# Kernel tuning notes

Hardware: AMD Instinct MI355X
Metric: run time of the kernel (lower is better)

## Reference

```python
import jax, jax.numpy as jnp
import numpy as np

GAMMA = 2.0  # init arg gamma
EPS = 1e-8   # torch F.cosine_similarity eps


def setup_inputs() -> dict:
    key = jax.random.key(0)
    k1, k2, k3 = jax.random.split(key, 3)
    B, C, H, W_ = 4, 256, 64, 64
    x = jax.random.normal(k1, (B, C, H, W_), dtype=jnp.float32)
    # 1x1 conv weight [out_c, in_c] and bias
    W = jax.random.normal(k2, (C, C), dtype=jnp.float32) * (1.0 / np.sqrt(C))
    b = jax.random.normal(k3, (C,), dtype=jnp.float32) * 0.01
    return {"x": x, "W": W, "b": b}


def reference(x, W, b):
    B, C, H, W_ = x.shape
    N = H * W_
    xf = x.reshape(B, C, N)                                    # [B,C,N]
    # cosine similarity across channel dim, with torch-style eps clamp
    norm = jnp.maximum(jnp.sqrt(jnp.sum(xf * xf, axis=1)), EPS)  # [B,N]
    xn = xf / norm[:, None, :]                                  # [B,C,N]
    sim = jnp.einsum('bcn,bcm->bnm', xn, xn)                    # [B,N,N]
    sim = jax.nn.relu(sim) ** GAMMA
    # 1x1 conv = per-pixel channel mixing
    t = jnp.einsum('oc,bchw->bohw', W, x) + b[None, :, None, None]
    tf = t.reshape(B, C, N)                                     # [B,C,N]
    # einsum 'b x y h w, b c h w -> b c x y'
    out = jnp.einsum('bnm,bcm->bcn', sim, tf)
    return out.reshape(B, C, H, W_)
```

## Files before the change

kernel.cpp:

```cpp
#include <hip/hip_runtime.h>
#include <stdint.h>

#define CC 256
#define NN 4096

typedef __attribute__((ext_vector_type(8))) short short8;
typedef __attribute__((ext_vector_type(4))) float floatx4;
typedef __attribute__((ext_vector_type(4))) unsigned int uint4v;
typedef __attribute__((ext_vector_type(2))) unsigned int uint2v;

__device__ __forceinline__ unsigned short f2bf(float f) {
    unsigned int u = __builtin_bit_cast(unsigned int, f);
    u = (u + 0x7FFFu + ((u >> 16) & 1u)) >> 16;
    return (unsigned short)u;
}

__device__ __forceinline__ floatx4 mfma16(short8 a, short8 b, floatx4 c) {
    return __builtin_amdgcn_mfma_f32_16x16x32_bf16(a, b, c, 0, 0, 0);
}

__device__ __forceinline__ int swz8(int row, int g) {
    return row * 256 + (((g ^ (row & 7)) & 31) << 3);
}

__global__ __launch_bounds__(256) void k_wcast(const float* __restrict__ Wm,
                                               unsigned short* __restrict__ wF) {
    int idx = blockIdx.x * 256 + threadIdx.x;
    int f = idx >> 6, lane = idx & 63;
    int ct = f >> 3, kk = f & 7;
    int l15 = lane & 15, q = lane >> 4;
    const float* src = Wm + (size_t)(16 * ct + l15) * CC + 32 * kk + 8 * q;
    floatx4 a = *(const floatx4*)src;
    floatx4 c = *(const floatx4*)(src + 4);
    unsigned int w0 = f2bf(a[0]) | ((unsigned int)f2bf(a[1]) << 16);
    unsigned int w1 = f2bf(a[2]) | ((unsigned int)f2bf(a[3]) << 16);
    unsigned int w2 = f2bf(c[0]) | ((unsigned int)f2bf(c[1]) << 16);
    unsigned int w3 = f2bf(c[2]) | ((unsigned int)f2bf(c[3]) << 16);
    uint4v p = {w0, w1, w2, w3};
    *(uint4v*)(wF + (size_t)f * 512 + lane * 8) = p;
}

__global__ __launch_bounds__(256) void k_trans(const float* __restrict__ x,
                                               unsigned short* __restrict__ xT,
                                               float* __restrict__ psum) {
    int blk = blockIdx.x;
    int b  = blk >> 8;
    int cc = (blk >> 6) & 3;
    int nc = blk & 63;
    int c0 = cc << 6, n0 = nc << 6;
    __shared__ float tile[64][65];
    __shared__ float red[4][64];
    int t = threadIdx.x;
    {
        int c   = t >> 2;
        int nn4 = (t & 3) << 4;
        const float* src = x + (size_t)(b * CC + c0 + c) * NN + n0 + nn4;
        #pragma unroll
        for (int j = 0; j < 16; j += 4) {
            floatx4 v = *(const floatx4*)(src + j);
            tile[c][nn4 + j + 0] = v[0];
            tile[c][nn4 + j + 1] = v[1];
            tile[c][nn4 + j + 2] = v[2];
            tile[c][nn4 + j + 3] = v[3];
        }
    }
    __syncthreads();
    {
        int n  = t >> 2;
        int ci = (t & 3) << 4;
        unsigned short* dst = xT + (size_t)(b * NN + n0 + n) * CC + c0 + ci;
        unsigned int w[8];
        #pragma unroll
        for (int j = 0; j < 8; ++j) {
            unsigned int lo = f2bf(tile[ci + 2 * j][n]);
            unsigned int hi = f2bf(tile[ci + 2 * j + 1][n]);
            w[j] = lo | (hi << 16);
        }
        uint4v w0 = {w[0], w[1], w[2], w[3]};
        uint4v w1 = {w[4], w[5], w[6], w[7]};
        *(uint4v*)(dst)     = w0;
        *(uint4v*)(dst + 8) = w1;
    }
    {
        int n  = t & 63;
        int cq = t >> 6;
        float ss = 0.f;
        #pragma unroll
        for (int i = 0; i < 16; ++i) {
            float v = tile[cq * 16 + i][n];
            ss = fmaf(v, v, ss);
        }
        red[cq][n] = ss;
    }
    __syncthreads();
    if (t < 64) {
        float s = red[0][t] + red[1][t] + red[2][t] + red[3][t];
        psum[((size_t)(b * 64 + nc) * 64 + t) * 4 + cc] = s;
    }
}

__global__ __launch_bounds__(256) void k_inv(const float* __restrict__ psum,
                                             float* __restrict__ invn) {
    int i = blockIdx.x * 256 + threadIdx.x;
    floatx4 p = *(const floatx4*)(psum + (size_t)i * 4);
    float ss = (p[0] + p[1]) + (p[2] + p[3]);
    invn[i] = 1.f / fmaxf(sqrtf(ss), 1e-8f);
}

__global__ __launch_bounds__(256) void k_gfrag(const unsigned short* __restrict__ xT,
                                               unsigned short* __restrict__ xG) {
    int blk = blockIdx.x;
    int b = blk >> 6, mt = blk & 63;
    __shared__ unsigned short tile[64 * 264];
    int t = threadIdx.x;
    const unsigned short* src = xT + (size_t)(b * NN + mt * 64) * CC;
    #pragma unroll
    for (int j = 0; j < 8; ++j) {
        int idx = j * 256 + t;
        int row = idx >> 5, g = idx & 31;
        uint4v v = *(const uint4v*)(src + (size_t)row * CC + g * 8);
        *(uint4v*)(tile + row * 264 + g * 8) = v;
    }
    __syncthreads();
    unsigned short* dst = xG + (size_t)(b * 64 + mt) * 16 * 1024;
    int lane = t & 63, l15 = lane & 15, q = lane >> 4;
    #pragma unroll
    for (int cc2 = 0; cc2 < 4; ++cc2) {
        int cct = (t >> 6) * 4 + cc2;
        #pragma unroll
        for (int kk2 = 0; kk2 < 2; ++kk2) {
            unsigned int w[4];
            #pragma unroll
            for (int j2 = 0; j2 < 4; ++j2) {
                unsigned int lo = tile[(32 * kk2 + 8 * q + 2 * j2) * 264 + 16 * cct + l15];
                unsigned int hi = tile[(32 * kk2 + 8 * q + 2 * j2 + 1) * 264 + 16 * cct + l15];
                w[j2] = lo | (hi << 16);
            }
            uint4v p = {w[0], w[1], w[2], w[3]};
            *(uint4v*)(dst + cct * 1024 + kk2 * 512 + lane * 8) = p;
        }
    }
}

__global__ __launch_bounds__(512, 2) void k_fused(
        const unsigned short* __restrict__ xT,
        const unsigned short* __restrict__ xG,
        const unsigned short* __restrict__ wF,
        const float* __restrict__ bias,
        const float* __restrict__ invn,
        float* __restrict__ out) {
    int blk = blockIdx.x;
    int b  = blk >> 6;
    int n0 = (blk & 63) << 6;
    int t  = threadIdx.x;
    int wv = t >> 6;
    int l15 = t & 15, q = (t & 63) >> 4;
    int ms = wv & 3;
    int np = wv >> 2;

    __shared__ unsigned short xm[64 * 256];
    __shared__ unsigned short pbuf[4][16 * 72];
    __shared__ unsigned short zbuf[64 * 264];
    __shared__ float spbuf2[4][64];

    const unsigned short* xTb = xT + (size_t)b * NN * CC;
    const unsigned short* xGb = xG + (size_t)b * 64 * 16 * 1024;
    const float* invb = invn + b * NN;

    short8 aq[2][8];
    #pragma unroll
    for (int s = 0; s < 2; ++s) {
        const unsigned short* p = xTb + (size_t)(n0 + 16 * (2 * np + s) + l15) * CC + q * 8;
        #pragma unroll
        for (int kk = 0; kk < 8; ++kk) aq[s][kk] = *(const short8*)(p + kk * 32);
    }
    float invq[2][4];
    #pragma unroll
    for (int s = 0; s < 2; ++s)
        #pragma unroll
        for (int i = 0; i < 4; ++i)
            invq[s][i] = invb[n0 + 16 * (2 * np + s) + q * 4 + i];

    floatx4 zero4 = {0.f, 0.f, 0.f, 0.f};
    floatx4 Zacc[2][4];
    #pragma unroll
    for (int ci = 0; ci < 2; ++ci)
        #pragma unroll
        for (int nqs = 0; nqs < 4; ++nqs) Zacc[ci][nqs] = zero4;
    float csum[2][4];
    #pragma unroll
    for (int s = 0; s < 2; ++s)
        #pragma unroll
        for (int i = 0; i < 4; ++i) csum[s][i] = 0.f;

    int srow = t >> 5;
    int sg   = t & 31;
    uint4v gx[4];
    #pragma unroll
    for (int j = 0; j < 4; ++j)
        gx[j] = *(const uint4v*)(xTb + (size_t)(j * 16 + srow) * CC + sg * 8);
    #pragma unroll
    for (int j = 0; j < 4; ++j)
        *(uint4v*)(xm + swz8(j * 16 + srow, sg)) = gx[j];
    __syncthreads();

    for (int it = 0; it < 64; ++it) {
        int m0 = it << 6;
        int m1 = (it < 63 ? (it + 1) : 63) << 6;
        #pragma unroll
        for (int j = 0; j < 4; ++j)
            gx[j] = *(const uint4v*)(xTb + (size_t)(m1 + j * 16 + srow) * CC + sg * 8);
        short8 xg[2][2];
        #pragma unroll
        for (int ci = 0; ci < 2; ++ci)
            #pragma unroll
            for (int kk2 = 0; kk2 < 2; ++kk2) {
                int cct = wv + 8 * ci;
                xg[ci][kk2] = *(const short8*)(xGb + (size_t)(it * 16 + cct) * 1024
                                               + kk2 * 512 + (t & 63) * 8);
            }
        float invm = invb[m0 + 16 * ms + l15];

        short8 bq[8];
        #pragma unroll
        for (int kk = 0; kk < 8; ++kk)
            bq[kk] = *(const short8*)(xm + swz8(16 * ms + l15, kk * 4 + q));
        floatx4 s0a = zero4, s0b = zero4, s1a = zero4, s1b = zero4;
        #pragma unroll
        for (int kk = 0; kk < 8; kk += 2) {
            s0a = mfma16(aq[0][kk],     bq[kk],     s0a);
            s1a = mfma16(aq[1][kk],     bq[kk],     s1a);
            s0b = mfma16(aq[0][kk + 1], bq[kk + 1], s0b);
            s1b = mfma16(aq[1][kk + 1], bq[kk + 1], s1b);
        }
        #pragma unroll
        for (int s = 0; s < 2; ++s) {
            floatx4 sv = (s == 0) ? (s0a + s0b) : (s1a + s1b);
            unsigned short* pw = &pbuf[2 * np + s][16 * ms + l15];
            #pragma unroll
            for (int i = 0; i < 4; ++i) {
                float v = sv[i] * (invq[s][i] * invm);
                v = fmaxf(v, 0.f);
                v = v * v;
                csum[s][i] += v;
                pw[(q * 4 + i) * 72] = f2bf(v);
            }
        }
        asm volatile("s_waitcnt lgkmcnt(0)\n\ts_barrier" ::: "memory");

        #pragma unroll
        for (int kk2 = 0; kk2 < 2; ++kk2)
            #pragma unroll
            for (int nqs = 0; nqs < 4; ++nqs) {
                short8 pbf = *(const short8*)(&pbuf[nqs][l15 * 72 + kk2 * 32 + q * 8]);
                Zacc[0][nqs] = mfma16(xg[0][kk2], pbf, Zacc[0][nqs]);
                Zacc[1][nqs] = mfma16(xg[1][kk2], pbf, Zacc[1][nqs]);
            }
        #pragma unroll
        for (int j = 0; j < 4; ++j)
            *(uint4v*)(xm + swz8(j * 16 + srow, sg)) = gx[j];
        asm volatile("s_waitcnt lgkmcnt(0)\n\ts_barrier" ::: "memory");
    }

    #pragma unroll
    for (int mask = 1; mask < 16; mask <<= 1)
        #pragma unroll
        for (int s = 0; s < 2; ++s)
            #pragma unroll
            for (int i = 0; i < 4; ++i)
                csum[s][i] += __shfl_xor(csum[s][i], mask, 64);

    __syncthreads();
    #pragma unroll
    for (int ci = 0; ci < 2; ++ci) {
        int cct = wv + 8 * ci;
        #pragma unroll
        for (int nqs = 0; nqs < 4; ++nqs)
            #pragma unroll
            for (int i = 0; i < 4; ++i)
                zbuf[(16 * nqs + l15) * 264 + 16 * cct + 4 * q + i] = f2bf(Zacc[ci][nqs][i]);
    }
    if (l15 == 0) {
        #pragma unroll
        for (int s = 0; s < 2; ++s)
            #pragma unroll
            for (int i = 0; i < 4; ++i)
                spbuf2[ms][16 * (2 * np + s) + 4 * q + i] = csum[s][i];
    }
    __syncthreads();

    float svals[4];
    #pragma unroll
    for (int nqs = 0; nqs < 4; ++nqs)
        svals[nqs] = spbuf2[0][16 * nqs + l15] + spbuf2[1][16 * nqs + l15]
                   + spbuf2[2][16 * nqs + l15] + spbuf2[3][16 * nqs + l15];

    float* ob = out + (size_t)b * CC * NN;
    floatx4 oa[2][4];
    #pragma unroll
    for (int ci = 0; ci < 2; ++ci) {
        int ct = wv + 8 * ci;
        floatx4 bv = *(const floatx4*)(bias + 16 * ct + 4 * q);
        #pragma unroll
        for (int nqs = 0; nqs < 4; ++nqs)
            #pragma unroll
            for (int i = 0; i < 4; ++i) oa[ci][nqs][i] = bv[i] * svals[nqs];
    }
    #pragma unroll
    for (int kk = 0; kk < 8; ++kk) {
        short8 wf0 = *(const short8*)(wF + (size_t)(wv * 8 + kk) * 512 + (t & 63) * 8);
        short8 wf1 = *(const short8*)(wF + (size_t)((wv + 8) * 8 + kk) * 512 + (t & 63) * 8);
        #pragma unroll
        for (int nqs = 0; nqs < 4; ++nqs) {
            short8 zf = *(const short8*)(&zbuf[(16 * nqs + l15) * 264 + 32 * kk + 8 * q]);
            oa[0][nqs] = mfma16(wf0, zf, oa[0][nqs]);
            oa[1][nqs] = mfma16(wf1, zf, oa[1][nqs]);
        }
    }
    #pragma unroll
    for (int ci = 0; ci < 2; ++ci) {
        int ct = wv + 8 * ci;
        #pragma unroll
        for (int nqs = 0; nqs < 4; ++nqs)
            #pragma unroll
            for (int i = 0; i < 4; ++i)
                ob[(size_t)(16 * ct + 4 * q + i) * NN + n0 + 16 * nqs + l15] = oa[ci][nqs][i];
    }
}

extern "C" void kernel_launch(void* const* d_in, const int* in_sizes, int n_in,
                              void* d_out, int out_size, void* d_ws, size_t ws_size,
                              hipStream_t stream) {
    const float* x    = (const float*)d_in[0];
    const float* Wm   = (const float*)d_in[1];
    const float* bias = (const float*)d_in[2];
    float* out = (float*)d_out;

    char* ws = (char*)d_ws;
    float* psum         = (float*)ws;
    float* invn         = (float*)(ws + 262144);
    unsigned short* xT  = (unsigned short*)(ws + 262144 + 65536);
    unsigned short* wF  = (unsigned short*)(ws + 262144 + 65536 + 8388608);
    unsigned short* xG  = (unsigned short*)(ws + 262144 + 65536 + 8388608 + 131072);

    k_wcast<<<32,   256, 0, stream>>>(Wm, wF);
    k_trans<<<1024, 256, 0, stream>>>(x, xT, psum);
    k_inv  <<<64,   256, 0, stream>>>(psum, invn);
    k_gfrag<<<256,  256, 0, stream>>>(xT, xG);
    k_fused<<<256,  512, 0, stream>>>(xT, xG, wF, bias, invn, out);
}
```

Measured before the change: 169.9 us.

## Emit MFMA-fragment layouts directly from transpose kernel and drop LDS staging loop

The transpose kernel now writes x in two pre-swizzled MFMA fragment layouts (xB for the similarity operand, xG for the aggregation operand), which removes the separate gfrag kernel. The weight cast is merged with the inverse-norm kernel, cutting five launches to three. In the fused kernel the per-iteration key tile is read straight from global memory in fragment order rather than staged through swizzled LDS, and pbuf is double-buffered. Together these remove one barrier and the LDS round trip per iteration. The cost is more global and L2 traffic for the key fragments and a larger workspace.

```diff
diff --git a/kernel.cpp b/kernel.cpp
--- a/kernel.cpp
+++ b/kernel.cpp
@@ -7,7 +7,6 @@
 typedef __attribute__((ext_vector_type(8))) short short8;
 typedef __attribute__((ext_vector_type(4))) float floatx4;
 typedef __attribute__((ext_vector_type(4))) unsigned int uint4v;
-typedef __attribute__((ext_vector_type(2))) unsigned int uint2v;
 
 __device__ __forceinline__ unsigned short f2bf(float f) {
     unsigned int u = __builtin_bit_cast(unsigned int, f);
@@ -19,29 +18,10 @@
     return __builtin_amdgcn_mfma_f32_16x16x32_bf16(a, b, c, 0, 0, 0);
 }
 
-__device__ __forceinline__ int swz8(int row, int g) {
-    return row * 256 + (((g ^ (row & 7)) & 31) << 3);
-}
-
-__global__ __launch_bounds__(256) void k_wcast(const float* __restrict__ Wm,
-                                               unsigned short* __restrict__ wF) {
-    int idx = blockIdx.x * 256 + threadIdx.x;
-    int f = idx >> 6, lane = idx & 63;
-    int ct = f >> 3, kk = f & 7;
-    int l15 = lane & 15, q = lane >> 4;
-    const float* src = Wm + (size_t)(16 * ct + l15) * CC + 32 * kk + 8 * q;
-    floatx4 a = *(const floatx4*)src;
-    floatx4 c = *(const floatx4*)(src + 4);
-    unsigned int w0 = f2bf(a[0]) | ((unsigned int)f2bf(a[1]) << 16);
-    unsigned int w1 = f2bf(a[2]) | ((unsigned int)f2bf(a[3]) << 16);
-    unsigned int w2 = f2bf(c[0]) | ((unsigned int)f2bf(c[1]) << 16);
-    unsigned int w3 = f2bf(c[2]) | ((unsigned int)f2bf(c[3]) << 16);
-    uint4v p = {w0, w1, w2, w3};
-    *(uint4v*)(wF + (size_t)f * 512 + lane * 8) = p;
-}
 
 __global__ __launch_bounds__(256) void k_trans(const float* __restrict__ x,
-                                               unsigned short* __restrict__ xT,
+                                               unsigned short* __restrict__ xB,
+                                               unsigned short* __restrict__ xG,
                                                float* __restrict__ psum) {
     int blk = blockIdx.x;
     int b  = blk >> 8;
@@ -65,21 +45,32 @@
         }
     }
     __syncthreads();
-    {
-        int n  = t >> 2;
-        int ci = (t & 3) << 4;
-        unsigned short* dst = xT + (size_t)(b * NN + n0 + n) * CC + c0 + ci;
-        unsigned int w[8];
-        #pragma unroll
-        for (int j = 0; j < 8; ++j) {
-            unsigned int lo = f2bf(tile[ci + 2 * j][n]);
-            unsigned int hi = f2bf(tile[ci + 2 * j + 1][n]);
+    int g = t >> 6, lane = t & 63, l15 = lane & 15, q = lane >> 4;
+    #pragma unroll
+    for (int kkl = 0; kkl < 2; ++kkl) {
+        unsigned int w[4];
+        #pragma unroll
+        for (int j = 0; j < 4; ++j) {
+            unsigned int lo = f2bf(tile[32 * kkl + 8 * q + 2 * j][16 * g + l15]);
+            unsigned int hi = f2bf(tile[32 * kkl + 8 * q + 2 * j + 1][16 * g + l15]);
             w[j] = lo | (hi << 16);
         }
-        uint4v w0 = {w[0], w[1], w[2], w[3]};
-        uint4v w1 = {w[4], w[5], w[6], w[7]};
-        *(uint4v*)(dst)     = w0;
-        *(uint4v*)(dst + 8) = w1;
+        uint4v p = {w[0], w[1], w[2], w[3]};
+        *(uint4v*)(xB + ((size_t)(b * 256 + (n0 >> 4) + g) * 8 + (c0 >> 5) + kkl) * 512
+                   + lane * 8) = p;
+    }
+    #pragma unroll
+    for (int kk2 = 0; kk2 < 2; ++kk2) {
+        unsigned int w[4];
+        #pragma unroll
+        for (int j = 0; j < 4; ++j) {
+            unsigned int lo = f2bf(tile[16 * g + l15][32 * kk2 + 8 * q + 2 * j]);
+            unsigned int hi = f2bf(tile[16 * g + l15][32 * kk2 + 8 * q + 2 * j + 1]);
+            w[j] = lo | (hi << 16);
+        }
+        uint4v p = {w[0], w[1], w[2], w[3]};
+        *(uint4v*)(xG + (size_t)(b * 64 + nc) * 16 * 1024
+                   + ((size_t)((c0 >> 4) + g)) * 1024 + kk2 * 512 + lane * 8) = p;
     }
     {
         int n  = t & 63;
@@ -99,51 +90,36 @@
     }
 }
 
-__global__ __launch_bounds__(256) void k_inv(const float* __restrict__ psum,
-                                             float* __restrict__ invn) {
-    int i = blockIdx.x * 256 + threadIdx.x;
-    floatx4 p = *(const floatx4*)(psum + (size_t)i * 4);
-    float ss = (p[0] + p[1]) + (p[2] + p[3]);
-    invn[i] = 1.f / fmaxf(sqrtf(ss), 1e-8f);
-}
-
-__global__ __launch_bounds__(256) void k_gfrag(const unsigned short* __restrict__ xT,
-                                               unsigned short* __restrict__ xG) {
-    int blk = blockIdx.x;
-    int b = blk >> 6, mt = blk & 63;
-    __shared__ unsigned short tile[64 * 264];
+__global__ __launch_bounds__(256) void k_invwcast(const float* __restrict__ psum,
+                                                  float* __restrict__ invn,
+                                                  const float* __restrict__ Wm,
+                                                  unsigned short* __restrict__ wF) {
+    int bid = blockIdx.x;
     int t = threadIdx.x;
-    const unsigned short* src = xT + (size_t)(b * NN + mt * 64) * CC;
-    #pragma unroll
-    for (int j = 0; j < 8; ++j) {
-        int idx = j * 256 + t;
-        int row = idx >> 5, g = idx & 31;
-        uint4v v = *(const uint4v*)(src + (size_t)row * CC + g * 8);
-        *(uint4v*)(tile + row * 264 + g * 8) = v;
-    }
-    __syncthreads();
-    unsigned short* dst = xG + (size_t)(b * 64 + mt) * 16 * 1024;
-    int lane = t & 63, l15 = lane & 15, q = lane >> 4;
-    #pragma unroll
-    for (int cc2 = 0; cc2 < 4; ++cc2) {
-        int cct = (t >> 6) * 4 + cc2;
-        #pragma unroll
-        for (int kk2 = 0; kk2 < 2; ++kk2) {
-            unsigned int w[4];
-            #pragma unroll
-            for (int j2 = 0; j2 < 4; ++j2) {
-                unsigned int lo = tile[(32 * kk2 + 8 * q + 2 * j2) * 264 + 16 * cct + l15];
-                unsigned int hi = tile[(32 * kk2 + 8 * q + 2 * j2 + 1) * 264 + 16 * cct + l15];
-                w[j2] = lo | (hi << 16);
-            }
-            uint4v p = {w[0], w[1], w[2], w[3]};
-            *(uint4v*)(dst + cct * 1024 + kk2 * 512 + lane * 8) = p;
-        }
+    if (bid < 64) {
+        int i = bid * 256 + t;
+        floatx4 p = *(const floatx4*)(psum + (size_t)i * 4);
+        float ss = (p[0] + p[1]) + (p[2] + p[3]);
+        invn[i] = 1.f / fmaxf(sqrtf(ss), 1e-8f);
+    } else {
+        int idx = (bid - 64) * 256 + t;
+        int f = idx >> 6, lane = idx & 63;
+        int ct = f >> 3, kk = f & 7;
+        int l15 = lane & 15, q = lane >> 4;
+        const float* src = Wm + (size_t)(16 * ct + l15) * CC + 32 * kk + 8 * q;
+        floatx4 a = *(const floatx4*)src;
+        floatx4 c = *(const floatx4*)(src + 4);
+        unsigned int w0 = f2bf(a[0]) | ((unsigned int)f2bf(a[1]) << 16);
+        unsigned int w1 = f2bf(a[2]) | ((unsigned int)f2bf(a[3]) << 16);
+        unsigned int w2 = f2bf(c[0]) | ((unsigned int)f2bf(c[1]) << 16);
+        unsigned int w3 = f2bf(c[2]) | ((unsigned int)f2bf(c[3]) << 16);
+        uint4v p = {w0, w1, w2, w3};
+        *(uint4v*)(wF + (size_t)f * 512 + lane * 8) = p;
     }
 }
 
 __global__ __launch_bounds__(512, 2) void k_fused(
-        const unsigned short* __restrict__ xT,
+        const unsigned short* __restrict__ xB,
         const unsigned short* __restrict__ xG,
         const unsigned short* __restrict__ wF,
         const float* __restrict__ bias,
@@ -153,27 +129,26 @@
     int b  = blk >> 6;
     int n0 = (blk & 63) << 6;
     int t  = threadIdx.x;
-    int wv = t >> 6;
-    int l15 = t & 15, q = (t & 63) >> 4;
+    int wv = t >> 6, lane = t & 63;
+    int l15 = lane & 15, q = lane >> 4;
     int ms = wv & 3;
     int np = wv >> 2;
 
-    __shared__ unsigned short xm[64 * 256];
-    __shared__ unsigned short pbuf[4][16 * 72];
+    __shared__ unsigned short pbuf[2][64 * 72];
     __shared__ unsigned short zbuf[64 * 264];
     __shared__ float spbuf2[4][64];
 
-    const unsigned short* xTb = xT + (size_t)b * NN * CC;
+    const unsigned short* xBb = xB + (size_t)b * 256 * 8 * 512;
     const unsigned short* xGb = xG + (size_t)b * 64 * 16 * 1024;
     const float* invb = invn + b * NN;
 
     short8 aq[2][8];
     #pragma unroll
-    for (int s = 0; s < 2; ++s) {
-        const unsigned short* p = xTb + (size_t)(n0 + 16 * (2 * np + s) + l15) * CC + q * 8;
-        #pragma unroll
-        for (int kk = 0; kk < 8; ++kk) aq[s][kk] = *(const short8*)(p + kk * 32);
-    }
+    for (int s = 0; s < 2; ++s)
+        #pragma unroll
+        for (int kk = 0; kk < 8; ++kk)
+            aq[s][kk] = *(const short8*)(xBb
+                + ((size_t)((n0 >> 4) + 2 * np + s) * 8 + kk) * 512 + lane * 8);
     float invq[2][4];
     #pragma unroll
     for (int s = 0; s < 2; ++s)
@@ -193,38 +168,23 @@
         #pragma unroll
         for (int i = 0; i < 4; ++i) csum[s][i] = 0.f;
 
-    int srow = t >> 5;
-    int sg   = t & 31;
-    uint4v gx[4];
-    #pragma unroll
-    for (int j = 0; j < 4; ++j)
-        gx[j] = *(const uint4v*)(xTb + (size_t)(j * 16 + srow) * CC + sg * 8);
-    #pragma unroll
-    for (int j = 0; j < 4; ++j)
-        *(uint4v*)(xm + swz8(j * 16 + srow, sg)) = gx[j];
-    __syncthreads();
-
     for (int it = 0; it < 64; ++it) {
+        unsigned short* pb = pbuf[it & 1];
         int m0 = it << 6;
-        int m1 = (it < 63 ? (it + 1) : 63) << 6;
-        #pragma unroll
-        for (int j = 0; j < 4; ++j)
-            gx[j] = *(const uint4v*)(xTb + (size_t)(m1 + j * 16 + srow) * CC + sg * 8);
+        short8 bq[8];
+        #pragma unroll
+        for (int kk = 0; kk < 8; ++kk)
+            bq[kk] = *(const short8*)(xBb
+                + ((size_t)(it * 4 + ms) * 8 + kk) * 512 + lane * 8);
         short8 xg[2][2];
         #pragma unroll
         for (int ci = 0; ci < 2; ++ci)
             #pragma unroll
-            for (int kk2 = 0; kk2 < 2; ++kk2) {
-                int cct = wv + 8 * ci;
-                xg[ci][kk2] = *(const short8*)(xGb + (size_t)(it * 16 + cct) * 1024
-                                               + kk2 * 512 + (t & 63) * 8);
-            }
+            for (int kk2 = 0; kk2 < 2; ++kk2)
+                xg[ci][kk2] = *(const short8*)(xGb
+                    + (size_t)(it * 16 + wv + 8 * ci) * 1024 + kk2 * 512 + lane * 8);
         float invm = invb[m0 + 16 * ms + l15];
 
-        short8 bq[8];
-        #pragma unroll
-        for (int kk = 0; kk < 8; ++kk)
-            bq[kk] = *(const short8*)(xm + swz8(16 * ms + l15, kk * 4 + q));
         floatx4 s0a = zero4, s0b = zero4, s1a = zero4, s1b = zero4;
         #pragma unroll
         for (int kk = 0; kk < 8; kk += 2) {
@@ -236,7 +196,7 @@
         #pragma unroll
         for (int s = 0; s < 2; ++s) {
             floatx4 sv = (s == 0) ? (s0a + s0b) : (s1a + s1b);
-            unsigned short* pw = &pbuf[2 * np + s][16 * ms + l15];
+            unsigned short* pw = pb + (16 * (2 * np + s)) * 72 + 16 * ms + l15;
             #pragma unroll
             for (int i = 0; i < 4; ++i) {
                 float v = sv[i] * (invq[s][i] * invm);
@@ -252,14 +212,11 @@
         for (int kk2 = 0; kk2 < 2; ++kk2)
             #pragma unroll
             for (int nqs = 0; nqs < 4; ++nqs) {
-                short8 pbf = *(const short8*)(&pbuf[nqs][l15 * 72 + kk2 * 32 + q * 8]);
+                short8 pbf = *(const short8*)(pb + (16 * nqs + l15) * 72
+                                              + kk2 * 32 + q * 8);
                 Zacc[0][nqs] = mfma16(xg[0][kk2], pbf, Zacc[0][nqs]);
                 Zacc[1][nqs] = mfma16(xg[1][kk2], pbf, Zacc[1][nqs]);
             }
-        #pragma unroll
-        for (int j = 0; j < 4; ++j)
-            *(uint4v*)(xm + swz8(j * 16 + srow, sg)) = gx[j];
-        asm volatile("s_waitcnt lgkmcnt(0)\n\ts_barrier" ::: "memory");
     }
 
     #pragma unroll
@@ -308,8 +265,8 @@
     }
     #pragma unroll
     for (int kk = 0; kk < 8; ++kk) {
-        short8 wf0 = *(const short8*)(wF + (size_t)(wv * 8 + kk) * 512 + (t & 63) * 8);
-        short8 wf1 = *(const short8*)(wF + (size_t)((wv + 8) * 8 + kk) * 512 + (t & 63) * 8);
+        short8 wf0 = *(const short8*)(wF + (size_t)(wv * 8 + kk) * 512 + lane * 8);
+        short8 wf1 = *(const short8*)(wF + (size_t)((wv + 8) * 8 + kk) * 512 + lane * 8);
         #pragma unroll
         for (int nqs = 0; nqs < 4; ++nqs) {
             short8 zf = *(const short8*)(&zbuf[(16 * nqs + l15) * 264 + 32 * kk + 8 * q]);
@@ -339,13 +296,11 @@
     char* ws = (char*)d_ws;
     float* psum         = (float*)ws;
     float* invn         = (float*)(ws + 262144);
-    unsigned short* xT  = (unsigned short*)(ws + 262144 + 65536);
-    unsigned short* wF  = (unsigned short*)(ws + 262144 + 65536 + 8388608);
-    unsigned short* xG  = (unsigned short*)(ws + 262144 + 65536 + 8388608 + 131072);
-
-    k_wcast<<<32,   256, 0, stream>>>(Wm, wF);
-    k_trans<<<1024, 256, 0, stream>>>(x, xT, psum);
-    k_inv  <<<64,   256, 0, stream>>>(psum, invn);
-    k_gfrag<<<256,  256, 0, stream>>>(xT, xG);
-    k_fused<<<256,  512, 0, stream>>>(xT, xG, wF, bias, invn, out);
-}
+    unsigned short* xB  = (unsigned short*)(ws + 262144 + 65536);
+    unsigned short* xG  = (unsigned short*)(ws + 262144 + 65536 + 8388608);
+    unsigned short* wF  = (unsigned short*)(ws + 262144 + 65536 + 2 * 8388608);
+
+    k_trans   <<<1024, 256, 0, stream>>>(x, xB, xG, psum);
+    k_invwcast<<<96,   256, 0, stream>>>(psum, invn, Wm, wF);
+    k_fused   <<<256,  512, 0, stream>>>(xB, xG, wF, bias, invn, out);
+}
```

Result: slower. 201.5 us (+18.6%).
